# Optimization experiments

Measured on AMD Instinct MI355X. Metric: run time of the kernel, lower is better.

Reference implementation:

```python
import jax, jax.numpy as jnp
import numpy as np

B, S, DIM, N_CONCEPTS, N_LAYERS = 4, 2048, 1024, 2048, 2


def _phase_linear(x, W, b):
    # x: [b,s,d_in,2]; same real linear applied to real and imag components
    return jnp.einsum('bsdp,od->bsop', x, W) + b[:, None]


def _phase_layernorm(x, gamma, beta, eps=1e-5):
    # per-component LayerNorm over the feature dim with shared affine params
    mu = x.mean(axis=-2, keepdims=True)
    var = x.var(axis=-2, keepdims=True)
    return (x - mu) / jnp.sqrt(var + eps) * gamma[:, None] + beta[:, None]


def setup_inputs() -> dict:
    key = jax.random.key(0)
    ks = jax.random.split(key, 8)
    x = jax.random.normal(ks[0], (B, S, DIM, 2), dtype=jnp.float32)
    concept_memory = jax.random.normal(ks[1], (N_CONCEPTS, DIM, 2), dtype=jnp.float32) * 0.02
    scale = 1.0 / np.sqrt(DIM)
    W_layers = jax.random.normal(ks[2], (N_LAYERS, DIM, DIM), dtype=jnp.float32) * scale
    b_layers = jnp.zeros((N_LAYERS, DIM), dtype=jnp.float32)
    gamma = jnp.ones((N_LAYERS, DIM), dtype=jnp.float32)
    beta = jnp.zeros((N_LAYERS, DIM), dtype=jnp.float32)
    W_out = jax.random.normal(ks[3], (DIM, DIM), dtype=jnp.float32) * scale
    b_out = jnp.zeros((DIM,), dtype=jnp.float32)
    g_out = jnp.ones((DIM,), dtype=jnp.float32)
    beta_out = jnp.zeros((DIM,), dtype=jnp.float32)
    return {"x": x, "concept_memory": concept_memory, "W_layers": W_layers,
            "b_layers": b_layers, "gamma": gamma, "beta": beta,
            "W_out": W_out, "b_out": b_out, "g_out": g_out, "beta_out": beta_out}


def reference(x, concept_memory, W_layers, b_layers, gamma, beta, W_out, b_out, g_out, beta_out):
    xr, xi = x[..., 0], x[..., 1]                       # [b,s,d]
    cr, ci = concept_memory[..., 0], concept_memory[..., 1]  # [n,d]
    # phase-coherence concept attention
    dot_real = jnp.einsum('bsd,nd->bsn', xr, cr) + jnp.einsum('bsd,nd->bsn', xi, ci)
    x_mag = jnp.sqrt((xr ** 2 + xi ** 2).sum(axis=-1, keepdims=True) + 1e-8)   # [b,s,1]
    c_mag = jnp.sqrt((cr ** 2 + ci ** 2).sum(axis=-1) + 1e-8)                  # [n]
    coherence = dot_real / (x_mag * c_mag[None, None, :] + 1e-8)
    concept_attn = jax.nn.softmax(coherence * 2.0, axis=-1)
    concept_retrieved = jnp.einsum('bsn,ndp->bsdp', concept_attn, concept_memory)
    h = x + concept_retrieved * 0.1
    # gated FFN blocks (eval mode: dropout off)
    for l in range(N_LAYERS):
        residual = h
        h = _phase_layernorm(h, gamma[l], beta[l])
        h = _phase_linear(h, W_layers[l], b_layers[l])
        h = jax.nn.gelu(h[..., 0:1], approximate=False) * h
        h = residual + h * 0.1
    out = _phase_layernorm(h, g_out, beta_out)
    out = _phase_linear(out, W_out, b_out)
    return out
```

## Files before the change

### kernel.cpp

```cpp
#include <hip/hip_runtime.h>
#include <hip/hip_bf16.h>

#define ROWS 8192
#define K2   2048
#define NCPT 2048
#define DIMD 1024

using short8 = __attribute__((ext_vector_type(8))) short;
using f32x4  = __attribute__((ext_vector_type(4))) float;

__device__ __forceinline__ unsigned short f2b(float f) {
  __hip_bfloat16 h = __float2bfloat16(f);
  return *reinterpret_cast<unsigned short*>(&h);
}
__device__ __forceinline__ float b2f(unsigned short u) {
  unsigned int x = ((unsigned int)u) << 16;
  return __uint_as_float(x);
}

__device__ __forceinline__ void store_bf16x8(unsigned short* dst, const float4& a, const float4& b) {
  union { unsigned short u[8]; uint4 q; } p;
  p.u[0]=f2b(a.x); p.u[1]=f2b(a.y); p.u[2]=f2b(a.z); p.u[3]=f2b(a.w);
  p.u[4]=f2b(b.x); p.u[5]=f2b(b.y); p.u[6]=f2b(b.z); p.u[7]=f2b(b.w);
  *reinterpret_cast<uint4*>(dst) = p.q;
}
__device__ __forceinline__ void store_bf16x4(unsigned short* dst, float a, float b, float c, float d) {
  union { unsigned short u[4]; uint2 q; } p;
  p.u[0]=f2b(a); p.u[1]=f2b(b); p.u[2]=f2b(c); p.u[3]=f2b(d);
  *reinterpret_cast<uint2*>(dst) = p.q;
}

__device__ __forceinline__ void async_lds16(const void* g, void* l) {
  __builtin_amdgcn_global_load_lds((__attribute__((address_space(1))) void*)g,
                                   (__attribute__((address_space(3))) void*)l, 16, 0, 0);
}

__global__ void cast_row_mag(const float* __restrict__ src, unsigned short* __restrict__ dst,
                             float* __restrict__ mag, int ncol) {
  __shared__ float sred[4];
  int row = blockIdx.x, t = threadIdx.x;
  const float* s = src + (size_t)row * ncol;
  unsigned short* d = dst + (size_t)row * ncol;
  float ss = 0.f;
  for (int i = t * 8; i < ncol; i += 2048) {
    float4 a = *(const float4*)(s + i);
    float4 b = *(const float4*)(s + i + 4);
    ss += a.x*a.x + a.y*a.y + a.z*a.z + a.w*a.w;
    ss += b.x*b.x + b.y*b.y + b.z*b.z + b.w*b.w;
    store_bf16x8(d + i, a, b);
  }
  int lane = t & 63, w = t >> 6;
  for (int o = 32; o; o >>= 1) ss += __shfl_down(ss, o);
  if (lane == 0) sred[w] = ss;
  __syncthreads();
  if (t == 0) mag[row] = sqrtf(sred[0] + sred[1] + sred[2] + sred[3] + 1e-8f);
}

__global__ void cast_f2b(const float* __restrict__ src, unsigned short* __restrict__ dst, int n) {
  int stride = gridDim.x * blockDim.x * 8;
  for (int i = (blockIdx.x * blockDim.x + threadIdx.x) * 8; i < n; i += stride) {
    float4 a = *(const float4*)(src + i);
    float4 b = *(const float4*)(src + i + 4);
    store_bf16x8(dst + i, a, b);
  }
}

__global__ void transpose_f2b(const float* __restrict__ src, unsigned short* __restrict__ dst, int n) {
  __shared__ float tile[32][33];
  int bx = blockIdx.x * 32;
  int by = blockIdx.y * 32;
  int tx = threadIdx.x & 31, ty = threadIdx.x >> 5;
  #pragma unroll
  for (int i = ty; i < 32; i += 8)
    tile[i][tx] = src[(size_t)(by + i) * n + bx + tx];
  __syncthreads();
  #pragma unroll
  for (int i = ty; i < 32; i += 8)
    dst[(size_t)(bx + i) * n + by + tx] = f2b(tile[tx][i]);
}

__global__ void softmax_attn(const unsigned short* __restrict__ logit, unsigned short* __restrict__ attn) {
  __shared__ float sred[4];
  int row = blockIdx.x, t = threadIdx.x;
  int lane = t & 63, w = t >> 6;
  const unsigned short* lr = logit + (size_t)row * NCPT + t * 8;
  short8 lv = *reinterpret_cast<const short8*>(lr);
  float l[8];
  #pragma unroll
  for (int i = 0; i < 8; ++i) l[i] = b2f((unsigned short)lv[i]);
  float m = l[0];
  #pragma unroll
  for (int i = 1; i < 8; ++i) m = fmaxf(m, l[i]);
  for (int o = 32; o; o >>= 1) m = fmaxf(m, __shfl_down(m, o));
  if (lane == 0) sred[w] = m;
  __syncthreads();
  m = fmaxf(fmaxf(sred[0], sred[1]), fmaxf(sred[2], sred[3]));
  __syncthreads();
  float e[8], s = 0.f;
  #pragma unroll
  for (int i = 0; i < 8; ++i) { e[i] = expf(l[i] - m); s += e[i]; }
  for (int o = 32; o; o >>= 1) s += __shfl_down(s, o);
  if (lane == 0) sred[w] = s;
  __syncthreads();
  s = sred[0] + sred[1] + sred[2] + sred[3];
  float inv = 1.f / s;
  float4 A = make_float4(e[0]*inv, e[1]*inv, e[2]*inv, e[3]*inv);
  float4 B = make_float4(e[4]*inv, e[5]*inv, e[6]*inv, e[7]*inv);
  store_bf16x8(attn + (size_t)row * NCPT + t * 8, A, B);
}

__global__ void phase_ln(const unsigned short* __restrict__ h, const float* __restrict__ gamma,
                         const float* __restrict__ beta, unsigned short* __restrict__ out) {
  __shared__ float4 s4[4];
  int bs = blockIdx.x, t = threadIdx.x;
  const unsigned short* hr = h + (size_t)bs * 2048 + t * 8;
  short8 hv = *reinterpret_cast<const short8*>(hr);
  float r0 = b2f((unsigned short)hv[0]), i0 = b2f((unsigned short)hv[1]);
  float r1 = b2f((unsigned short)hv[2]), i1 = b2f((unsigned short)hv[3]);
  float r2 = b2f((unsigned short)hv[4]), i2 = b2f((unsigned short)hv[5]);
  float r3 = b2f((unsigned short)hv[6]), i3 = b2f((unsigned short)hv[7]);
  float4 s;
  s.x = r0 + r1 + r2 + r3;
  s.y = r0*r0 + r1*r1 + r2*r2 + r3*r3;
  s.z = i0 + i1 + i2 + i3;
  s.w = i0*i0 + i1*i1 + i2*i2 + i3*i3;
  int lane = t & 63, w = t >> 6;
  for (int o = 32; o; o >>= 1) {
    s.x += __shfl_down(s.x, o); s.y += __shfl_down(s.y, o);
    s.z += __shfl_down(s.z, o); s.w += __shfl_down(s.w, o);
  }
  if (lane == 0) s4[w] = s;
  __syncthreads();
  float4 T = s4[0];
  #pragma unroll
  for (int i = 1; i < 4; ++i) { T.x += s4[i].x; T.y += s4[i].y; T.z += s4[i].z; T.w += s4[i].w; }
  const float invd = 1.f / 1024.f;
  float mu_r = T.x * invd, var_r = T.y * invd - mu_r * mu_r;
  float mu_i = T.z * invd, var_i = T.w * invd - mu_i * mu_i;
  float is_r = 1.f / sqrtf(var_r + 1e-5f);
  float is_i = 1.f / sqrtf(var_i + 1e-5f);
  float4 g = *(const float4*)(gamma + t * 4);
  float4 b = *(const float4*)(beta + t * 4);
  unsigned short* o0 = out + (size_t)(2 * bs) * 1024 + t * 4;
  unsigned short* o1 = out + (size_t)(2 * bs + 1) * 1024 + t * 4;
  store_bf16x4(o0, (r0-mu_r)*is_r*g.x + b.x, (r1-mu_r)*is_r*g.y + b.y,
                   (r2-mu_r)*is_r*g.z + b.z, (r3-mu_r)*is_r*g.w + b.w);
  store_bf16x4(o1, (i0-mu_i)*is_i*g.x + b.x, (i1-mu_i)*is_i*g.y + b.y,
                   (i2-mu_i)*is_i*g.z + b.z, (i3-mu_i)*is_i*g.w + b.w);
}

template <int EPI>
__global__ __launch_bounds__(512, 2) void gemm256(
    const unsigned short* __restrict__ A, const unsigned short* __restrict__ B,
    int M, int N, int K, void* __restrict__ Cv, const float* __restrict__ aux,
    const float* __restrict__ aux2, const unsigned short* __restrict__ auxb) {
  __shared__ char lds[131072];
  const int t = threadIdx.x;
  const int l = t & 63;
  const int wid = t >> 6;
  const int wm = wid >> 2, wn = wid & 3;

  const int nwg = gridDim.x * gridDim.y;
  int bid = blockIdx.y * gridDim.x + blockIdx.x;
  const int chunk = nwg >> 3;
  bid = (bid & 7) * chunk + (bid >> 3);
  const int row0 = (bid / gridDim.x) * 256;
  const int col0 = (bid % gridDim.x) * 256;

  const int NT = K >> 6;
  const int l15 = l & 15, l7 = l & 7, lk = l >> 4;

  f32x4 acc[8][4] = {};
  short8 afA[4][2];
  short8 bfA[2][2];
  short8 bfB[2][2];

  auto stage = [&](const unsigned short* gmat, int tileRow, int kcol, char* region) {
    const int rsub = t >> 3;
    const int csw = ((t & 7) ^ (rsub & 7)) << 3;
    const unsigned short* g0 = gmat + (size_t)(tileRow + rsub) * K + kcol + csw;
    async_lds16(g0, region + (t & ~63) * 16);
    async_lds16(g0 + (size_t)64 * K, region + 8192 + (t & ~63) * 16);
  };

  auto rdA = [&](const char* base, int m, int kh) -> short8 {
    const int r = wm * 64 + m * 16 + l15;
    const int sp = ((((kh << 2) | lk) ^ l7) << 4);
    return *reinterpret_cast<const short8*>(base + r * 128 + sp);
  };
  auto rdB = [&](const char* base, int n, int kh) -> short8 {
    const int r = wn * 32 + n * 16 + l15;
    const int sp = ((((kh << 2) | lk) ^ l7) << 4);
    return *reinterpret_cast<const short8*>(base + r * 128 + sp);
  };

  stage(A, row0,       0, lds + 0);
  stage(A, row0 + 128, 0, lds + 16384);
  stage(B, col0,       0, lds + 32768);
  stage(B, col0 + 128, 0, lds + 49152);
  if (NT > 1) {
    stage(A, row0,       64, lds + 65536 + 0);
    stage(A, row0 + 128, 64, lds + 65536 + 16384);
    stage(B, col0,       64, lds + 65536 + 32768);
    stage(B, col0 + 128, 64, lds + 65536 + 49152);
    asm volatile("s_waitcnt vmcnt(8)" ::: "memory");
  } else {
    asm volatile("s_waitcnt vmcnt(0)" ::: "memory");
  }
  __builtin_amdgcn_s_barrier();
  asm volatile("" ::: "memory");

  #pragma unroll
  for (int n = 0; n < 2; ++n)
    #pragma unroll
    for (int kh = 0; kh < 2; ++kh)
      bfA[n][kh] = rdB(lds + 32768, n, kh);

  for (int tk = 0; tk < NT; ++tk) {
    char* bufC = lds + (tk & 1) * 65536;
    char* bufN = lds + (((tk + 1) & 1) * 65536);
    const bool pf = (tk + 2 < NT);
    const int kpf = (tk + 2) * 64;

    #pragma unroll
    for (int m = 0; m < 4; ++m)
      #pragma unroll
      for (int kh = 0; kh < 2; ++kh)
        afA[m][kh] = rdA(bufC + 0, m, kh);
    __builtin_amdgcn_s_setprio(1);
    #pragma unroll
    for (int kh = 0; kh < 2; ++kh)
      #pragma unroll
      for (int m = 0; m < 4; ++m)
        #pragma unroll
        for (int n = 0; n < 2; ++n)
          acc[m][n] = __builtin_amdgcn_mfma_f32_16x16x32_bf16(afA[m][kh], bfA[n][kh], acc[m][n], 0, 0, 0);
    __builtin_amdgcn_s_setprio(0);
    #pragma unroll
    for (int n = 0; n < 2; ++n)
      #pragma unroll
      for (int kh = 0; kh < 2; ++kh)
        bfB[n][kh] = rdB(bufC + 49152, n, kh);
    asm volatile("" ::: "memory");
    __builtin_amdgcn_s_barrier();
    asm volatile("" ::: "memory");

    __builtin_amdgcn_s_setprio(1);
    #pragma unroll
    for (int kh = 0; kh < 2; ++kh)
      #pragma unroll
      for (int m = 0; m < 4; ++m)
        #pragma unroll
        for (int n = 0; n < 2; ++n)
          acc[m][n + 2] = __builtin_amdgcn_mfma_f32_16x16x32_bf16(afA[m][kh], bfB[n][kh], acc[m][n + 2], 0, 0, 0);
    __builtin_amdgcn_s_setprio(0);
    if (pf) {
      stage(A, row0, kpf, bufC + 0);
      stage(B, col0, kpf, bufC + 32768);
    }
    asm volatile("" ::: "memory");
    __builtin_amdgcn_s_barrier();
    asm volatile("" ::: "memory");

    #pragma unroll
    for (int m = 0; m < 4; ++m)
      #pragma unroll
      for (int kh = 0; kh < 2; ++kh)
        afA[m][kh] = rdA(bufC + 16384, m, kh);
    __builtin_amdgcn_s_setprio(1);
    #pragma unroll
    for (int kh = 0; kh < 2; ++kh)
      #pragma unroll
      for (int m = 0; m < 4; ++m)
        #pragma unroll
        for (int n = 0; n < 2; ++n)
          acc[m + 4][n] = __builtin_amdgcn_mfma_f32_16x16x32_bf16(afA[m][kh], bfA[n][kh], acc[m + 4][n], 0, 0, 0);
    __builtin_amdgcn_s_setprio(0);
    if (pf) stage(B, col0 + 128, kpf, bufC + 49152);
    asm volatile("" ::: "memory");
    __builtin_amdgcn_s_barrier();
    asm volatile("" ::: "memory");

    __builtin_amdgcn_s_setprio(1);
    #pragma unroll
    for (int kh = 0; kh < 2; ++kh)
      #pragma unroll
      for (int m = 0; m < 4; ++m)
        #pragma unroll
        for (int n = 0; n < 2; ++n)
          acc[m + 4][n + 2] = __builtin_amdgcn_mfma_f32_16x16x32_bf16(afA[m][kh], bfB[n][kh], acc[m + 4][n + 2], 0, 0, 0);
    __builtin_amdgcn_s_setprio(0);
    if (pf) stage(A, row0 + 128, kpf, bufC + 16384);
    if (tk + 1 < NT) {
      #pragma unroll
      for (int n = 0; n < 2; ++n)
        #pragma unroll
        for (int kh = 0; kh < 2; ++kh)
          bfA[n][kh] = rdB(bufN + 32768, n, kh);
    }
    if (pf) {
      asm volatile("s_waitcnt vmcnt(4)" ::: "memory");
    } else {
      asm volatile("s_waitcnt vmcnt(0)" ::: "memory");
    }
    __builtin_amdgcn_s_barrier();
    asm volatile("" ::: "memory");
  }
  asm volatile("s_waitcnt vmcnt(0)" ::: "memory");

  const int cr = lk * 4;
  #pragma unroll
  for (int m = 0; m < 8; ++m) {
    const int gr = row0 + ((m >> 2) << 7) + wm * 64 + ((m & 3) << 4) + cr;
    #pragma unroll
    for (int n = 0; n < 4; ++n) {
      const int gc = col0 + ((n >> 1) << 7) + wn * 32 + ((n & 1) << 4) + l15;
      if constexpr (EPI == 0) {
        unsigned short* C = (unsigned short*)Cv;
        const float cm_ = aux2[gc];
        #pragma unroll
        for (int j = 0; j < 4; ++j) {
          const int r = gr + j;
          float v = 2.f * acc[m][n][j] / (aux[r] * cm_ + 1e-8f);
          C[(size_t)r * N + gc] = f2b(v);
        }
      } else if constexpr (EPI == 1) {
        unsigned short* C = (unsigned short*)Cv;
        #pragma unroll
        for (int j = 0; j < 4; ++j) {
          const int r = gr + j;
          C[(size_t)r * N + gc] = f2b(b2f(auxb[(size_t)r * N + gc]) + 0.1f * acc[m][n][j]);
        }
      } else if constexpr (EPI == 2) {
        unsigned short* C = (unsigned short*)Cv;
        const float bb = aux[gc];
        #pragma unroll
        for (int jj = 0; jj < 2; ++jj) {
          const int r = gr + jj * 2;
          float re = acc[m][n][jj * 2] + bb;
          float im = acc[m][n][jj * 2 + 1] + bb;
          float g = 0.5f * re * (1.f + erff(re * 0.70710678118654752440f));
          size_t idx = (size_t)(r >> 1) * 2048 + (size_t)gc * 2;
          unsigned int hv = *(unsigned int*)(C + idx);
          float hx = b2f((unsigned short)(hv & 0xffff));
          float hy = b2f((unsigned short)(hv >> 16));
          hx += 0.1f * g * re;
          hy += 0.1f * g * im;
          unsigned int packed = (unsigned int)f2b(hx) | ((unsigned int)f2b(hy) << 16);
          *(unsigned int*)(C + idx) = packed;
        }
      } else {
        float* C = (float*)Cv;
        #pragma unroll
        for (int j = 0; j < 4; ++j) {
          const int r = gr + j;
          C[(size_t)(r >> 1) * 2048 + (size_t)gc * 2 + (r & 1)] = acc[m][n][j] + aux[gc];
        }
      }
    }
  }
}

extern "C" void kernel_launch(void* const* d_in, const int* in_sizes, int n_in,
                              void* d_out, int out_size, void* d_ws, size_t ws_size,
                              hipStream_t stream) {
  const float* x     = (const float*)d_in[0];
  const float* cm    = (const float*)d_in[1];
  const float* Wl    = (const float*)d_in[2];
  const float* bl    = (const float*)d_in[3];
  const float* gamma = (const float*)d_in[4];
  const float* beta  = (const float*)d_in[5];
  const float* Wo    = (const float*)d_in[6];
  const float* bo    = (const float*)d_in[7];
  const float* go    = (const float*)d_in[8];
  const float* bto   = (const float*)d_in[9];
  float* out = (float*)d_out;

  char* p = (char*)d_ws;
  unsigned short* x_bf = (unsigned short*)p; p += (size_t)ROWS * K2 * 2;
  unsigned short* c_bf = (unsigned short*)p; p += (size_t)NCPT * K2 * 2;
  unsigned short* c_T  = (unsigned short*)p; p += (size_t)K2 * NCPT * 2;
  unsigned short* w_bf = (unsigned short*)p; p += (size_t)3 * 1024 * 1024 * 2;
  float* x_mag = (float*)p; p += (size_t)ROWS * 4;
  float* c_mag = (float*)p; p += (size_t)NCPT * 4;
  unsigned short* dot_bf = (unsigned short*)p; p += (size_t)ROWS * NCPT * 2;
  unsigned short* attn   = (unsigned short*)p; p += (size_t)ROWS * NCPT * 2;
  unsigned short* h      = (unsigned short*)p; p += (size_t)ROWS * K2 * 2;
  unsigned short* ln_bf = attn;

  cast_row_mag<<<ROWS, 256, 0, stream>>>(x, x_bf, x_mag, K2);
  cast_row_mag<<<NCPT, 256, 0, stream>>>(cm, c_bf, c_mag, K2);
  transpose_f2b<<<dim3(64, 64), 256, 0, stream>>>(cm, c_T, 2048);
  cast_f2b<<<1024, 256, 0, stream>>>(Wl, w_bf, 2 * 1024 * 1024);
  cast_f2b<<<512, 256, 0, stream>>>(Wo, w_bf + 2 * 1024 * 1024, 1024 * 1024);

  gemm256<0><<<dim3(NCPT / 256, ROWS / 256), 512, 0, stream>>>(
      x_bf, c_bf, ROWS, NCPT, K2, dot_bf, x_mag, c_mag, nullptr);
  softmax_attn<<<ROWS, 256, 0, stream>>>(dot_bf, attn);
  gemm256<1><<<dim3(K2 / 256, ROWS / 256), 512, 0, stream>>>(
      attn, c_T, ROWS, K2, NCPT, h, nullptr, nullptr, x_bf);

  for (int l = 0; l < 2; ++l) {
    phase_ln<<<ROWS, 256, 0, stream>>>(h, gamma + l * 1024, beta + l * 1024, ln_bf);
    gemm256<2><<<dim3(DIMD / 256, 2 * ROWS / 256), 512, 0, stream>>>(
        ln_bf, w_bf + (size_t)l * 1024 * 1024, 2 * ROWS, DIMD, DIMD, h, bl + l * 1024, nullptr, nullptr);
  }

  phase_ln<<<ROWS, 256, 0, stream>>>(h, go, bto, ln_bf);
  gemm256<3><<<dim3(DIMD / 256, 2 * ROWS / 256), 512, 0, stream>>>(
      ln_bf, w_bf + 2 * 1024 * 1024, 2 * ROWS, DIMD, DIMD, out, bo, nullptr, nullptr);
}
```

Baseline: 363.6 us.

## Restructure GEMM main loop to double-buffer register fragments and overlap LDS reads

Reorganizes the four-quadrant MFMA loop so A and B fragments are held in two register sets (a0/a1, b0/b1). LDS reads for the next quadrant or next K-tile are issued before or alongside the current MFMAs, and global-to-LDS prefetch stages are interleaved differently. The goal is to hide LDS read latency behind matrix work and spread global loads across the loop. In exchange it uses more VGPRs, which could lower occupancy, and the prologue now waits for all loads before starting.

Result: slower. 382.1 us (+5.1%).

```diff
diff --git a/kernel.cpp b/kernel.cpp
--- a/kernel.cpp
+++ b/kernel.cpp
@@ -171,9 +171,7 @@
   const int l15 = l & 15, l7 = l & 7, lk = l >> 4;
 
   f32x4 acc[8][4] = {};
-  short8 afA[4][2];
-  short8 bfA[2][2];
-  short8 bfB[2][2];
+  short8 a0[4][2], a1[4][2], b0[2][2], b1[2][2];
 
   auto stage = [&](const unsigned short* gmat, int tileRow, int kcol, char* region) {
     const int rsub = t >> 3;
@@ -203,30 +201,55 @@
     stage(A, row0 + 128, 64, lds + 65536 + 16384);
     stage(B, col0,       64, lds + 65536 + 32768);
     stage(B, col0 + 128, 64, lds + 65536 + 49152);
-    asm volatile("s_waitcnt vmcnt(8)" ::: "memory");
-  } else {
-    asm volatile("s_waitcnt vmcnt(0)" ::: "memory");
-  }
+  }
+  asm volatile("s_waitcnt vmcnt(0)" ::: "memory");
   __builtin_amdgcn_s_barrier();
   asm volatile("" ::: "memory");
 
   #pragma unroll
+  for (int m = 0; m < 4; ++m)
+    #pragma unroll
+    for (int kh = 0; kh < 2; ++kh)
+      a0[m][kh] = rdA(lds + 0, m, kh);
+  #pragma unroll
   for (int n = 0; n < 2; ++n)
     #pragma unroll
     for (int kh = 0; kh < 2; ++kh)
-      bfA[n][kh] = rdB(lds + 32768, n, kh);
+      b0[n][kh] = rdB(lds + 32768, n, kh);
 
   for (int tk = 0; tk < NT; ++tk) {
     char* bufC = lds + (tk & 1) * 65536;
     char* bufN = lds + (((tk + 1) & 1) * 65536);
     const bool pf = (tk + 2 < NT);
+    const bool nx = (tk + 1 < NT);
     const int kpf = (tk + 2) * 64;
 
     #pragma unroll
+    for (int n = 0; n < 2; ++n)
+      #pragma unroll
+      for (int kh = 0; kh < 2; ++kh)
+        b1[n][kh] = rdB(bufC + 49152, n, kh);
+    asm volatile("s_waitcnt lgkmcnt(4)" ::: "memory");
+    if (pf) stage(A, row0, kpf, bufC + 0);
+    __builtin_amdgcn_s_setprio(1);
+    #pragma unroll
+    for (int kh = 0; kh < 2; ++kh)
+      #pragma unroll
+      for (int m = 0; m < 4; ++m)
+        #pragma unroll
+        for (int n = 0; n < 2; ++n)
+          acc[m][n] = __builtin_amdgcn_mfma_f32_16x16x32_bf16(a0[m][kh], b0[n][kh], acc[m][n], 0, 0, 0);
+    __builtin_amdgcn_s_setprio(0);
+    asm volatile("" ::: "memory");
+    __builtin_amdgcn_s_barrier();
+    asm volatile("" ::: "memory");
+
+    #pragma unroll
     for (int m = 0; m < 4; ++m)
       #pragma unroll
       for (int kh = 0; kh < 2; ++kh)
-        afA[m][kh] = rdA(bufC + 0, m, kh);
+        a1[m][kh] = rdA(bufC + 16384, m, kh);
+    if (pf) stage(B, col0, kpf, bufC + 32768);
     __builtin_amdgcn_s_setprio(1);
     #pragma unroll
     for (int kh = 0; kh < 2; ++kh)
@@ -234,17 +257,20 @@
       for (int m = 0; m < 4; ++m)
         #pragma unroll
         for (int n = 0; n < 2; ++n)
-          acc[m][n] = __builtin_amdgcn_mfma_f32_16x16x32_bf16(afA[m][kh], bfA[n][kh], acc[m][n], 0, 0, 0);
+          acc[m][n + 2] = __builtin_amdgcn_mfma_f32_16x16x32_bf16(a0[m][kh], b1[n][kh], acc[m][n + 2], 0, 0, 0);
     __builtin_amdgcn_s_setprio(0);
-    #pragma unroll
-    for (int n = 0; n < 2; ++n)
-      #pragma unroll
-      for (int kh = 0; kh < 2; ++kh)
-        bfB[n][kh] = rdB(bufC + 49152, n, kh);
     asm volatile("" ::: "memory");
     __builtin_amdgcn_s_barrier();
     asm volatile("" ::: "memory");
 
+    if (nx) {
+      #pragma unroll
+      for (int m = 0; m < 4; ++m)
+        #pragma unroll
+        for (int kh = 0; kh < 2; ++kh)
+          a0[m][kh] = rdA(bufN + 0, m, kh);
+    }
+    if (pf) stage(B, col0 + 128, kpf, bufC + 49152);
     __builtin_amdgcn_s_setprio(1);
     #pragma unroll
     for (int kh = 0; kh < 2; ++kh)
@@ -252,57 +278,35 @@
       for (int m = 0; m < 4; ++m)
         #pragma unroll
         for (int n = 0; n < 2; ++n)
-          acc[m][n + 2] = __builtin_amdgcn_mfma_f32_16x16x32_bf16(afA[m][kh], bfB[n][kh], acc[m][n + 2], 0, 0, 0);
+          acc[m + 4][n] = __builtin_amdgcn_mfma_f32_16x16x32_bf16(a1[m][kh], b0[n][kh], acc[m + 4][n], 0, 0, 0);
     __builtin_amdgcn_s_setprio(0);
-    if (pf) {
-      stage(A, row0, kpf, bufC + 0);
-      stage(B, col0, kpf, bufC + 32768);
-    }
     asm volatile("" ::: "memory");
     __builtin_amdgcn_s_barrier();
     asm volatile("" ::: "memory");
 
-    #pragma unroll
-    for (int m = 0; m < 4; ++m)
-      #pragma unroll
-      for (int kh = 0; kh < 2; ++kh)
-        afA[m][kh] = rdA(bufC + 16384, m, kh);
-    __builtin_amdgcn_s_setprio(1);
-    #pragma unroll
-    for (int kh = 0; kh < 2; ++kh)
-      #pragma unroll
-      for (int m = 0; m < 4; ++m)
-        #pragma unroll
-        for (int n = 0; n < 2; ++n)
-          acc[m + 4][n] = __builtin_amdgcn_mfma_f32_16x16x32_bf16(afA[m][kh], bfA[n][kh], acc[m + 4][n], 0, 0, 0);
-    __builtin_amdgcn_s_setprio(0);
-    if (pf) stage(B, col0 + 128, kpf, bufC + 49152);
-    asm volatile("" ::: "memory");
-    __builtin_amdgcn_s_barrier();
-    asm volatile("" ::: "memory");
-
-    __builtin_amdgcn_s_setprio(1);
-    #pragma unroll
-    for (int kh = 0; kh < 2; ++kh)
-      #pragma unroll
-      for (int m = 0; m < 4; ++m)
-        #pragma unroll
-        for (int n = 0; n < 2; ++n)
-          acc[m + 4][n + 2] = __builtin_amdgcn_mfma_f32_16x16x32_bf16(afA[m][kh], bfB[n][kh], acc[m + 4][n + 2], 0, 0, 0);
-    __builtin_amdgcn_s_setprio(0);
-    if (pf) stage(A, row0 + 128, kpf, bufC + 16384);
-    if (tk + 1 < NT) {
+    if (nx) {
       #pragma unroll
       for (int n = 0; n < 2; ++n)
         #pragma unroll
         for (int kh = 0; kh < 2; ++kh)
-          bfA[n][kh] = rdB(bufN + 32768, n, kh);
+          b0[n][kh] = rdB(bufN + 32768, n, kh);
     }
     if (pf) {
+      stage(A, row0 + 128, kpf, bufC + 16384);
       asm volatile("s_waitcnt vmcnt(4)" ::: "memory");
     } else {
       asm volatile("s_waitcnt vmcnt(0)" ::: "memory");
     }
+    __builtin_amdgcn_s_setprio(1);
+    #pragma unroll
+    for (int kh = 0; kh < 2; ++kh)
+      #pragma unroll
+      for (int m = 0; m < 4; ++m)
+        #pragma unroll
+        for (int n = 0; n < 2; ++n)
+          acc[m + 4][n + 2] = __builtin_amdgcn_mfma_f32_16x16x32_bf16(a1[m][kh], b1[n][kh], acc[m + 4][n + 2], 0, 0, 0);
+    __builtin_amdgcn_s_setprio(0);
+    asm volatile("" ::: "memory");
     __builtin_amdgcn_s_barrier();
     asm volatile("" ::: "memory");
   }
```

## Restructure GEMM main loop into eight-phase pipeline with finer-grained async staging

Applied to the files above, without the earlier changes.

Replaces the four-phase per-K-tile loop with a two-tile unrolled loop of eight phases. Each phase loads A and B fragments for one half-K slice, issues one async global-to-LDS stage, synchronises, then runs 16 MFMAs. The prologue now preloads only one extra subtile instead of a full second buffer. The goal is to spread global loads evenly across compute phases and shrink the fragment register footprint, at the cost of more barriers per K tile and carefully tuned vmcnt waits that could be wrong.

New measurement: 372.0 us. 2.3% more time.

```diff
diff --git a/kernel.cpp b/kernel.cpp
--- a/kernel.cpp
+++ b/kernel.cpp
@@ -149,6 +149,42 @@
                    (i2-mu_i)*is_i*g.z + b.z, (i3-mu_i)*is_i*g.w + b.w);
 }
 
+#define GPHASE(BUFX, RH, KH, READB, STAGE_STMT, CHK_STMT)                      \
+  {                                                                            \
+    _Pragma("unroll")                                                          \
+    for (int mf = 0; mf < 4; ++mf)                                             \
+      a_[mf] = *reinterpret_cast<const short8*>(                               \
+          (BUFX) + (RH) * 16384 + (wm * 64 + mf * 16 + l15) * 128 +            \
+          (((((KH) << 2) | lk) ^ l7) << 4));                                   \
+    if (READB) {                                                               \
+      _Pragma("unroll")                                                        \
+      for (int nf = 0; nf < 2; ++nf) {                                         \
+        b_[nf] = *reinterpret_cast<const short8*>(                             \
+            (BUFX) + 32768 + (wn * 32 + nf * 16 + l15) * 128 +                 \
+            (((((KH) << 2) | lk) ^ l7) << 4));                                 \
+        b_[nf + 2] = *reinterpret_cast<const short8*>(                         \
+            (BUFX) + 49152 + (wn * 32 + nf * 16 + l15) * 128 +                 \
+            (((((KH) << 2) | lk) ^ l7) << 4));                                 \
+      }                                                                        \
+    }                                                                          \
+    STAGE_STMT;                                                                \
+    asm volatile("" ::: "memory");                                             \
+    __builtin_amdgcn_s_barrier();                                              \
+    asm volatile("" ::: "memory");                                             \
+    __builtin_amdgcn_s_setprio(1);                                             \
+    _Pragma("unroll")                                                          \
+    for (int mf = 0; mf < 4; ++mf)                                             \
+      _Pragma("unroll")                                                        \
+      for (int nf = 0; nf < 4; ++nf)                                           \
+        acc[(RH) * 4 + mf][nf] = __builtin_amdgcn_mfma_f32_16x16x32_bf16(      \
+            a_[mf], b_[nf], acc[(RH) * 4 + mf][nf], 0, 0, 0);                  \
+    __builtin_amdgcn_s_setprio(0);                                             \
+    CHK_STMT;                                                                  \
+    asm volatile("" ::: "memory");                                             \
+    __builtin_amdgcn_s_barrier();                                              \
+    asm volatile("" ::: "memory");                                             \
+  }
+
 template <int EPI>
 __global__ __launch_bounds__(512, 2) void gemm256(
     const unsigned short* __restrict__ A, const unsigned short* __restrict__ B,
@@ -171,9 +207,10 @@
   const int l15 = l & 15, l7 = l & 7, lk = l >> 4;
 
   f32x4 acc[8][4] = {};
-  short8 afA[4][2];
-  short8 bfA[2][2];
-  short8 bfB[2][2];
+  short8 a_[4], b_[4];
+
+  char* const bufE = lds;
+  char* const bufO = lds + 65536;
 
   auto stage = [&](const unsigned short* gmat, int tileRow, int kcol, char* region) {
     const int rsub = t >> 3;
@@ -183,128 +220,52 @@
     async_lds16(g0 + (size_t)64 * K, region + 8192 + (t & ~63) * 16);
   };
 
-  auto rdA = [&](const char* base, int m, int kh) -> short8 {
-    const int r = wm * 64 + m * 16 + l15;
-    const int sp = ((((kh << 2) | lk) ^ l7) << 4);
-    return *reinterpret_cast<const short8*>(base + r * 128 + sp);
-  };
-  auto rdB = [&](const char* base, int n, int kh) -> short8 {
-    const int r = wn * 32 + n * 16 + l15;
-    const int sp = ((((kh << 2) | lk) ^ l7) << 4);
-    return *reinterpret_cast<const short8*>(base + r * 128 + sp);
-  };
-
-  stage(A, row0,       0, lds + 0);
-  stage(A, row0 + 128, 0, lds + 16384);
-  stage(B, col0,       0, lds + 32768);
-  stage(B, col0 + 128, 0, lds + 49152);
+  stage(A, row0,       0, bufE + 0);
+  stage(A, row0 + 128, 0, bufE + 16384);
+  stage(B, col0,       0, bufE + 32768);
+  stage(B, col0 + 128, 0, bufE + 49152);
   if (NT > 1) {
-    stage(A, row0,       64, lds + 65536 + 0);
-    stage(A, row0 + 128, 64, lds + 65536 + 16384);
-    stage(B, col0,       64, lds + 65536 + 32768);
-    stage(B, col0 + 128, 64, lds + 65536 + 49152);
-    asm volatile("s_waitcnt vmcnt(8)" ::: "memory");
+    stage(A, row0, 64, bufO + 0);
+    asm volatile("s_waitcnt vmcnt(2)" ::: "memory");
   } else {
     asm volatile("s_waitcnt vmcnt(0)" ::: "memory");
   }
   __builtin_amdgcn_s_barrier();
   asm volatile("" ::: "memory");
 
-  #pragma unroll
-  for (int n = 0; n < 2; ++n)
-    #pragma unroll
-    for (int kh = 0; kh < 2; ++kh)
-      bfA[n][kh] = rdB(lds + 32768, n, kh);
-
-  for (int tk = 0; tk < NT; ++tk) {
-    char* bufC = lds + (tk & 1) * 65536;
-    char* bufN = lds + (((tk + 1) & 1) * 65536);
-    const bool pf = (tk + 2 < NT);
-    const int kpf = (tk + 2) * 64;
-
-    #pragma unroll
-    for (int m = 0; m < 4; ++m)
-      #pragma unroll
-      for (int kh = 0; kh < 2; ++kh)
-        afA[m][kh] = rdA(bufC + 0, m, kh);
-    __builtin_amdgcn_s_setprio(1);
-    #pragma unroll
-    for (int kh = 0; kh < 2; ++kh)
-      #pragma unroll
-      for (int m = 0; m < 4; ++m)
-        #pragma unroll
-        for (int n = 0; n < 2; ++n)
-          acc[m][n] = __builtin_amdgcn_mfma_f32_16x16x32_bf16(afA[m][kh], bfA[n][kh], acc[m][n], 0, 0, 0);
-    __builtin_amdgcn_s_setprio(0);
-    #pragma unroll
-    for (int n = 0; n < 2; ++n)
-      #pragma unroll
-      for (int kh = 0; kh < 2; ++kh)
-        bfB[n][kh] = rdB(bufC + 49152, n, kh);
-    asm volatile("" ::: "memory");
-    __builtin_amdgcn_s_barrier();
-    asm volatile("" ::: "memory");
-
-    __builtin_amdgcn_s_setprio(1);
-    #pragma unroll
-    for (int kh = 0; kh < 2; ++kh)
-      #pragma unroll
-      for (int m = 0; m < 4; ++m)
-        #pragma unroll
-        for (int n = 0; n < 2; ++n)
-          acc[m][n + 2] = __builtin_amdgcn_mfma_f32_16x16x32_bf16(afA[m][kh], bfB[n][kh], acc[m][n + 2], 0, 0, 0);
-    __builtin_amdgcn_s_setprio(0);
-    if (pf) {
-      stage(A, row0, kpf, bufC + 0);
-      stage(B, col0, kpf, bufC + 32768);
-    }
-    asm volatile("" ::: "memory");
-    __builtin_amdgcn_s_barrier();
-    asm volatile("" ::: "memory");
-
-    #pragma unroll
-    for (int m = 0; m < 4; ++m)
-      #pragma unroll
-      for (int kh = 0; kh < 2; ++kh)
-        afA[m][kh] = rdA(bufC + 16384, m, kh);
-    __builtin_amdgcn_s_setprio(1);
-    #pragma unroll
-    for (int kh = 0; kh < 2; ++kh)
-      #pragma unroll
-      for (int m = 0; m < 4; ++m)
-        #pragma unroll
-        for (int n = 0; n < 2; ++n)
-          acc[m + 4][n] = __builtin_amdgcn_mfma_f32_16x16x32_bf16(afA[m][kh], bfA[n][kh], acc[m + 4][n], 0, 0, 0);
-    __builtin_amdgcn_s_setprio(0);
-    if (pf) stage(B, col0 + 128, kpf, bufC + 49152);
-    asm volatile("" ::: "memory");
-    __builtin_amdgcn_s_barrier();
-    asm volatile("" ::: "memory");
-
-    __builtin_amdgcn_s_setprio(1);
-    #pragma unroll
-    for (int kh = 0; kh < 2; ++kh)
-      #pragma unroll
-      for (int m = 0; m < 4; ++m)
-        #pragma unroll
-        for (int n = 0; n < 2; ++n)
-          acc[m + 4][n + 2] = __builtin_amdgcn_mfma_f32_16x16x32_bf16(afA[m][kh], bfB[n][kh], acc[m + 4][n + 2], 0, 0, 0);
-    __builtin_amdgcn_s_setprio(0);
-    if (pf) stage(A, row0 + 128, kpf, bufC + 16384);
-    if (tk + 1 < NT) {
-      #pragma unroll
-      for (int n = 0; n < 2; ++n)
-        #pragma unroll
-        for (int kh = 0; kh < 2; ++kh)
-          bfA[n][kh] = rdB(bufN + 32768, n, kh);
-    }
-    if (pf) {
-      asm volatile("s_waitcnt vmcnt(4)" ::: "memory");
-    } else {
-      asm volatile("s_waitcnt vmcnt(0)" ::: "memory");
-    }
-    __builtin_amdgcn_s_barrier();
-    asm volatile("" ::: "memory");
+  for (int e = 0; e < NT; e += 2) {
+    const int o64 = (e + 1) * 64;
+    const int k2 = (e + 2) * 64;
+    const int k3 = (e + 3) * 64;
+    const bool s4 = (e + 2 < NT);
+    const bool s8 = (e + 3 < NT);
+
+    GPHASE(bufE, 0, 0, true,
+           { stage(B, col0, o64, bufO + 32768); },
+           { asm volatile("s_waitcnt vmcnt(4)" ::: "memory"); });
+    GPHASE(bufE, 1, 0, false,
+           { stage(B, col0 + 128, o64, bufO + 49152); },
+           {});
+    GPHASE(bufE, 0, 1, true,
+           { stage(A, row0 + 128, o64, bufO + 16384); },
+           {});
+    GPHASE(bufE, 1, 1, false,
+           { if (s4) stage(A, row0, k2, bufE + 0); },
+           { if (s4) { asm volatile("s_waitcnt vmcnt(4)" ::: "memory"); }
+             else    { asm volatile("s_waitcnt vmcnt(0)" ::: "memory"); } });
+    GPHASE(bufO, 0, 0, true,
+           { if (s4) stage(B, col0, k2, bufE + 32768); },
+           { if (s4) { asm volatile("s_waitcnt vmcnt(4)" ::: "memory"); }
+             else    { asm volatile("s_waitcnt vmcnt(0)" ::: "memory"); } });
+    GPHASE(bufO, 1, 0, false,
+           { if (s4) stage(B, col0 + 128, k2, bufE + 49152); },
+           {});
+    GPHASE(bufO, 0, 1, true,
+           { if (s4) stage(A, row0 + 128, k2, bufE + 16384); },
+           {});
+    GPHASE(bufO, 1, 1, false,
+           { if (s8) stage(A, row0, k3, bufO + 0); },
+           { if (s4) { asm volatile("s_waitcnt vmcnt(4)" ::: "memory"); } });
   }
   asm volatile("s_waitcnt vmcnt(0)" ::: "memory");
 
```
